# Performance work log

Measured on AMD Instinct MI355X. Metric: run time of the kernel, lower is better.

## Reference

```python
import jax, jax.numpy as jnp
import numpy as np

B, L, H, M = 8, 512, 768, 383
N = M + 1  # +1 dummy epsilon mention
NEG = -10000.0


def _lin(x, W, b):
    return x @ W.T + b


def setup_inputs() -> dict:
    key = jax.random.key(0)
    ks = jax.random.split(key, 26)
    s = 0.02
    inp = {}
    inp["sequence_output"] = jax.random.normal(ks[0], (B, L, H), jnp.float32)
    inp["speaker_emb"] = jax.random.normal(ks[1], (400, H), jnp.float32) * s
    inp["dummy_emb"] = jax.random.normal(ks[2], (1, H), jnp.float32) * s
    inp["W_pair1"] = jax.random.normal(ks[3], (H, 2 * H), jnp.float32) * s
    inp["b_pair1"] = jnp.zeros((H,), jnp.float32)
    inp["W_pair2"] = jax.random.normal(ks[4], (H // 2, H), jnp.float32) * s
    inp["b_pair2"] = jnp.zeros((H // 2,), jnp.float32)
    inp["W_pair3"] = jax.random.normal(ks[5], (1, H // 2), jnp.float32) * s
    inp["b_pair3"] = jnp.zeros((1,), jnp.float32)
    inp["W_m1"] = jax.random.normal(ks[6], (H // 2, H), jnp.float32) * s
    inp["b_m1"] = jnp.zeros((H // 2,), jnp.float32)
    inp["W_m2"] = jax.random.normal(ks[7], (H // 4, H // 2), jnp.float32) * s
    inp["b_m2"] = jnp.zeros((H // 4,), jnp.float32)
    inp["W_m3"] = jax.random.normal(ks[8], (1, H // 4), jnp.float32) * s
    inp["b_m3"] = jnp.zeros((1,), jnp.float32)
    inp["W_c1"] = jax.random.normal(ks[9], (H // 2, H), jnp.float32) * s
    inp["b_c1"] = jnp.zeros((H // 2,), jnp.float32)
    inp["W_c2"] = jax.random.normal(ks[10], (18, H // 2), jnp.float32) * s
    inp["b_c2"] = jnp.zeros((18,), jnp.float32)
    inp["mentions_seg"] = jax.random.randint(ks[11], (M,), 0, B, jnp.int32)
    inp["mention_start"] = jax.random.randint(ks[12], (M,), 0, L, jnp.int32)
    inp["mention_end"] = jax.random.randint(ks[13], (M,), 0, L, jnp.int32)
    inp["speaker_ids"] = jax.random.randint(ks[14], (B, L), 0, 400, jnp.int32)
    second = jnp.arange(1, N, dtype=jnp.int32)  # each real mention is a 'second' exactly once
    first = jax.random.randint(ks[15], (M,), 0, N, jnp.int32) % second  # antecedent strictly before
    inp["link_first"] = first
    inp["link_second"] = second
    inp["character_label"] = jax.random.randint(ks[16], (M,), 0, 18, jnp.int32)
    return inp


def reference(sequence_output, speaker_emb, dummy_emb,
              W_pair1, b_pair1, W_pair2, b_pair2, W_pair3, b_pair3,
              W_m1, b_m1, W_m2, b_m2, W_m3, b_m3,
              W_c1, b_c1, W_c2, b_c2,
              mentions_seg, mention_start, mention_end, speaker_ids,
              link_first, link_second, character_label):
    relu = jax.nn.relu
    # gather mention boundary + speaker reps: [M, H]
    start_rep = sequence_output[mentions_seg, mention_start]
    end_rep = sequence_output[mentions_seg, mention_end]
    spk_rep = speaker_emb[speaker_ids[mentions_seg, mention_start]]
    mention_reps = start_rep + end_rep + spk_rep
    # character linking head: [M, 18]
    char_logits = _lin(relu(_lin(mention_reps, W_c1, b_c1)), W_c2, b_c2)
    # prepend dummy epsilon mention: [N, H]
    all_reps = jnp.concatenate([dummy_emb, mention_reps], axis=0)
    # pairwise MLP; pair[i, j] = MLP(cat(rep_j, rep_i)). Split W_pair1 to avoid [N,N,2H] concat.
    Wa, Wb = W_pair1[:, :H], W_pair1[:, H:]
    A = all_reps @ Wa.T  # contribution of 'first' (column j)
    Bm = all_reps @ Wb.T  # contribution of 'second' (row i)
    h1 = relu(A[None, :, :] + Bm[:, None, :] + b_pair1)  # [N, N, H]
    h2 = relu(jnp.einsum('ijk,hk->ijh', h1, W_pair2) + b_pair2)  # [N, N, H/2]
    pair_scores = jnp.einsum('ijh,oh->ij', h2, W_pair3) + b_pair3[0]  # [N, N]
    # unary mention score: [N]
    ms = (_lin(relu(_lin(relu(_lin(all_reps, W_m1, b_m1)), W_m2, b_m2)), W_m3, b_m3))[:, 0]
    mask = jnp.triu(jnp.ones((N, N), jnp.float32), k=0) * NEG
    mention_scores = pair_scores + ms[None, :] + ms[:, None] + mask
    # linking loss via row-softmax and link gathers
    sm = jax.nn.softmax(mention_scores, axis=1)
    lik = sm[link_second, link_first]  # [num_links]
    col_sum = jnp.zeros((N,), sm.dtype).at[link_second].add(lik)
    nll = -jnp.sum(jnp.log(col_sum[1:]))
    # character cross-entropy (sum reduction)
    logp = jax.nn.log_softmax(char_logits, axis=1)
    ce = -jnp.sum(jnp.take_along_axis(logp, character_label[:, None], axis=1))
    return nll + ce


if __name__ == '__main__':
    out = reference(**setup_inputs())
    print(out)
```

## Files before the change

### kernel.cpp

```cpp
#include <hip/hip_runtime.h>

typedef __bf16 bf16x8 __attribute__((ext_vector_type(8)));
typedef float f32x4 __attribute__((ext_vector_type(4)));

#define WS_S       0
#define WS_ALLREPS 0
#define WS_APRIME  301056
#define WS_BMAT    595968
#define WS_RELUM1  890880
#define WS_RELUC1  1038336
#define WS_MS      1185792
#define WS_W2BF    1186176

#define NPAIR 2352
#define NMS   384
#define NCE   383
#define SLAB  75264

#define SWZ(row,c) (((row)<<2) + ((c) ^ (((row)>>1)&3)))

__device__ __forceinline__ bf16x8 cvt8(float4 a, float4 b) {
  bf16x8 v;
  v[0]=(__bf16)a.x; v[1]=(__bf16)a.y; v[2]=(__bf16)a.z; v[3]=(__bf16)a.w;
  v[4]=(__bf16)b.x; v[5]=(__bf16)b.y; v[6]=(__bf16)b.z; v[7]=(__bf16)b.w;
  return v;
}

__global__ __launch_bounds__(256) void k_build(
    const float* __restrict__ seq, const float* __restrict__ spk_emb,
    const float* __restrict__ dummy, const float* __restrict__ W2,
    const int* __restrict__ seg, const int* __restrict__ mstart,
    const int* __restrict__ mend, const int* __restrict__ spk_ids,
    float* __restrict__ all_reps, __bf16* __restrict__ W2bf,
    float* __restrict__ out) {
  int r = blockIdx.x, t = threadIdx.x;
  if (r < 384) {
    if (r == 0) {
      if (t == 0) out[0] = 0.f;
      #pragma unroll
      for (int e = 0; e < 3; ++e) { int k = t + 256*e; all_reps[k] = dummy[k]; }
    } else {
      int m = r - 1;
      int sg = seg[m], st = mstart[m], en = mend[m];
      int sp = spk_ids[sg*512 + st];
      const float* p1 = seq + (size_t)(sg*512 + st)*768;
      const float* p2 = seq + (size_t)(sg*512 + en)*768;
      const float* p3 = spk_emb + (size_t)sp*768;
      #pragma unroll
      for (int e = 0; e < 3; ++e) { int k = t + 256*e; all_reps[r*768+k] = p1[k]+p2[k]+p3[k]; }
    }
  } else {
    int h = r - 384;
    #pragma unroll
    for (int e = 0; e < 3; ++e) { int k = t + 256*e; W2bf[h*768+k] = (__bf16)W2[h*768+k]; }
  }
}

__global__ __launch_bounds__(256) void k_gemmB(
    const float* __restrict__ reps, const float* __restrict__ W1,
    const float* __restrict__ Wm1, const float* __restrict__ Wc1,
    const float* __restrict__ b1, const float* __restrict__ bm1, const float* __restrict__ bc1,
    float* __restrict__ Aprime, float* __restrict__ Bmat,
    float* __restrict__ relu_m1, float* __restrict__ relu_c1) {
  __shared__ bf16x8 lA[2][256];
  __shared__ bf16x8 lB[2][512];
  int nt = blockIdx.x;
  int m0 = blockIdx.y * 64;
  int t = threadIdx.x;
  const float* src; int stride, coloff;
  if (nt < 6)       { src = W1  + (size_t)(nt*128)*1536;      stride = 1536; coloff = 0;   }
  else if (nt < 12) { src = W1  + (size_t)((nt-6)*128)*1536;  stride = 1536; coloff = 768; }
  else if (nt < 15) { src = Wm1 + (size_t)((nt-12)*128)*768;  stride = 768;  coloff = 0;   }
  else              { src = Wc1 + (size_t)((nt-15)*128)*768;  stride = 768;  coloff = 0;   }

  int w = t>>6, l = t&63;
  int wm = w&1, wn = w>>1;
  int lr = l&15, lg = l>>4;

  int p = t>>2, q = t&3;
  const float* pa  = reps + (size_t)(m0+p)*768 + q*8;
  const float* pb0 = src + (size_t)p*stride + coloff + q*8;
  const float* pb1 = src + (size_t)(p+64)*stride + coloff + q*8;
  int ia  = SWZ(p, q);
  int ib0 = SWZ(p, q);
  int ib1 = SWZ(p+64, q);

  float4 a0, a1, b0, b1v, c0, c1v;
  #define G_LOADG(k0) { \
    a0  = *(const float4*)(pa  + (k0)); a1  = *(const float4*)(pa  + (k0) + 4); \
    b0  = *(const float4*)(pb0 + (k0)); b1v = *(const float4*)(pb0 + (k0) + 4); \
    c0  = *(const float4*)(pb1 + (k0)); c1v = *(const float4*)(pb1 + (k0) + 4); }
  #define G_WRITEB(buf) { \
    lA[buf][ia]  = cvt8(a0, a1); \
    lB[buf][ib0] = cvt8(b0, b1v); \
    lB[buf][ib1] = cvt8(c0, c1v); }

  G_LOADG(0);
  G_WRITEB(0);

  f32x4 acc[2][4] = {};
  int cur = 0;

  for (int ks = 0; ks < 24; ++ks) {
    __syncthreads();
    if (ks < 23) G_LOADG((ks+1)*32);
    bf16x8 af[2], bfr[4];
    #pragma unroll
    for (int fa = 0; fa < 2; ++fa) { int row = wm*32 + fa*16 + lr; af[fa] = lA[cur][SWZ(row, lg)]; }
    #pragma unroll
    for (int fb = 0; fb < 4; ++fb) { int row = wn*64 + fb*16 + lr; bfr[fb] = lB[cur][SWZ(row, lg)]; }
    __builtin_amdgcn_s_setprio(1);
    #pragma unroll
    for (int fa = 0; fa < 2; ++fa)
      #pragma unroll
      for (int fb = 0; fb < 4; ++fb)
        acc[fa][fb] = __builtin_amdgcn_mfma_f32_16x16x32_bf16(af[fa], bfr[fb], acc[fa][fb], 0, 0, 0);
    __builtin_amdgcn_s_setprio(0);
    if (ks < 23) G_WRITEB(cur^1);
    cur ^= 1;
  }

  #pragma unroll
  for (int fa = 0; fa < 2; ++fa) {
    #pragma unroll
    for (int fb = 0; fb < 4; ++fb) {
      #pragma unroll
      for (int reg = 0; reg < 4; ++reg) {
        int m = m0 + wm*32 + fa*16 + lg*4 + reg;
        int nl = wn*64 + fb*16 + lr;
        float v = acc[fa][fb][reg];
        if (nt < 6)       { int n = nt*128 + nl;      Aprime[m*768+n]  = v + b1[n]; }
        else if (nt < 12) { int n = (nt-6)*128 + nl;  Bmat[m*768+n]    = v; }
        else if (nt < 15) { int n = (nt-12)*128 + nl; relu_m1[m*384+n] = fmaxf(v + bm1[n], 0.f); }
        else              { int n = (nt-15)*128 + nl; relu_c1[m*384+n] = fmaxf(v + bc1[n], 0.f); }
      }
    }
  }
}

__global__ __launch_bounds__(128, 2) void k_mega(
    const float* __restrict__ Aprime, const float* __restrict__ Bmat,
    const __bf16* __restrict__ W2bf, const float* __restrict__ b2,
    const float* __restrict__ w3, float* __restrict__ S,
    const float* __restrict__ relu_m1, const float* __restrict__ Wm2,
    const float* __restrict__ bm2, const float* __restrict__ Wm3,
    const float* __restrict__ bm3, float* __restrict__ msv,
    const float* __restrict__ relu_c1, const float* __restrict__ Wc2,
    const float* __restrict__ bc2, const int* __restrict__ label,
    float* __restrict__ out) {
  __shared__ char smem[32768];
  int bx = blockIdx.x, t = threadIdx.x;

  if (bx < NPAIR) {
    bf16x8 (*lA)[256] = (bf16x8 (*)[256])smem;
    bf16x8 (*lB)[768] = (bf16x8 (*)[768])(smem + 8192);
    int tile = bx >> 1, hh = bx & 1;
    int ib = (int)((__fsqrt_rn(8.0f*tile + 1.0f) - 1.0f) * 0.5f);
    while ((ib+1)*(ib+2)/2 <= tile) ++ib;
    while (ib*(ib+1)/2 > tile) --ib;
    int jb = tile - ib*(ib+1)/2;
    int i0 = ib*8, j0 = jb*8;
    int h0 = hh*192;

    int w = t>>6, l = t&63;
    int lr = l&15, lg = l>>4;

    int p = t>>1, qb = (t&1)*2;
    const float* pArow = Aprime + (size_t)(j0 + (p&7))*768 + qb*8;
    const float* pBrow = Bmat   + (size_t)(i0 + (p>>3))*768 + qb*8;
    int idxA0 = SWZ(p, qb), idxA1 = SWZ(p, qb+1);
    const __bf16* pW[6]; int idxW[6];
    #pragma unroll
    for (int e = 0; e < 6; ++e) {
      int c6 = t + 128*e, row = c6>>2, qq = c6&3;
      pW[e] = W2bf + (size_t)(h0 + row)*768 + qq*8;
      idxW[e] = SWZ(row, qq);
    }

    float4 ga0, ga1, ga2, ga3, gb0, gb1, gb2, gb3;
    bf16x8 gw0, gw1, gw2, gw3, gw4, gw5;

    #define LOADG(k0) { \
      ga0 = *(const float4*)(pArow + (k0));     ga1 = *(const float4*)(pArow + (k0) + 4); \
      ga2 = *(const float4*)(pArow + (k0) + 8); ga3 = *(const float4*)(pArow + (k0) + 12); \
      gb0 = *(const float4*)(pBrow + (k0));     gb1 = *(const float4*)(pBrow + (k0) + 4); \
      gb2 = *(const float4*)(pBrow + (k0) + 8); gb3 = *(const float4*)(pBrow + (k0) + 12); \
      gw0 = *(const bf16x8*)(pW[0] + (k0)); gw1 = *(const bf16x8*)(pW[1] + (k0)); \
      gw2 = *(const bf16x8*)(pW[2] + (k0)); gw3 = *(const bf16x8*)(pW[3] + (k0)); \
      gw4 = *(const bf16x8*)(pW[4] + (k0)); gw5 = *(const bf16x8*)(pW[5] + (k0)); }

    #define WRITEB(buf) { \
      float4 r0, r1, r2, r3; \
      r0.x = fmaxf(ga0.x + gb0.x, 0.f); r0.y = fmaxf(ga0.y + gb0.y, 0.f); \
      r0.z = fmaxf(ga0.z + gb0.z, 0.f); r0.w = fmaxf(ga0.w + gb0.w, 0.f); \
      r1.x = fmaxf(ga1.x + gb1.x, 0.f); r1.y = fmaxf(ga1.y + gb1.y, 0.f); \
      r1.z = fmaxf(ga1.z + gb1.z, 0.f); r1.w = fmaxf(ga1.w + gb1.w, 0.f); \
      r2.x = fmaxf(ga2.x + gb2.x, 0.f); r2.y = fmaxf(ga2.y + gb2.y, 0.f); \
      r2.z = fmaxf(ga2.z + gb2.z, 0.f); r2.w = fmaxf(ga2.w + gb2.w, 0.f); \
      r3.x = fmaxf(ga3.x + gb3.x, 0.f); r3.y = fmaxf(ga3.y + gb3.y, 0.f); \
      r3.z = fmaxf(ga3.z + gb3.z, 0.f); r3.w = fmaxf(ga3.w + gb3.w, 0.f); \
      lA[buf][idxA0] = cvt8(r0, r1); \
      lA[buf][idxA1] = cvt8(r2, r3); \
      lB[buf][idxW[0]] = gw0; lB[buf][idxW[1]] = gw1; lB[buf][idxW[2]] = gw2; \
      lB[buf][idxW[3]] = gw3; lB[buf][idxW[4]] = gw4; lB[buf][idxW[5]] = gw5; }

    LOADG(0);
    WRITEB(0);

    f32x4 acc[4][6] = {};
    int cur = 0;

    for (int ks = 0; ks < 24; ++ks) {
      __syncthreads();
      if (ks < 23) LOADG((ks+1)*32);
      bf16x8 af[4], bfr[6];
      #pragma unroll
      for (int fp = 0; fp < 4; ++fp) { int row = fp*16 + lr; af[fp] = lA[cur][SWZ(row, lg)]; }
      #pragma unroll
      for (int fh = 0; fh < 6; ++fh) { int row = w*96 + fh*16 + lr; bfr[fh] = lB[cur][SWZ(row, lg)]; }
      __builtin_amdgcn_s_setprio(1);
      #pragma unroll
      for (int fp = 0; fp < 4; ++fp)
        #pragma unroll
        for (int fh = 0; fh < 6; ++fh)
          acc[fp][fh] = __builtin_amdgcn_mfma_f32_16x16x32_bf16(af[fp], bfr[fh], acc[fp][fh], 0, 0, 0);
      __builtin_amdgcn_s_setprio(0);
      if (ks < 23) WRITEB(cur^1);
      cur ^= 1;
    }

    float sacc[4][4] = {};
    #pragma unroll
    for (int fh = 0; fh < 6; ++fh) {
      int hcol = h0 + w*96 + fh*16 + lr;
      float bb = b2[hcol], ww = w3[hcol];
      #pragma unroll
      for (int fp = 0; fp < 4; ++fp)
        #pragma unroll
        for (int reg = 0; reg < 4; ++reg)
          sacc[fp][reg] += fmaxf(acc[fp][fh][reg] + bb, 0.f) * ww;
    }
    float* Sp = S + (size_t)(hh*2 + w)*SLAB + tile*64;
    #pragma unroll
    for (int fp = 0; fp < 4; ++fp) {
      #pragma unroll
      for (int reg = 0; reg < 4; ++reg) {
        float v = sacc[fp][reg];
        v += __shfl_xor(v, 1); v += __shfl_xor(v, 2);
        v += __shfl_xor(v, 4); v += __shfl_xor(v, 8);
        if (lr == 0) Sp[fp*16 + lg*4 + reg] = v;
      }
    }
  } else if (bx < NPAIR + NMS) {
    float* xs = (float*)smem;
    __shared__ float part[2];
    int r = bx - NPAIR;
    const float4* srcv = (const float4*)(relu_m1 + (size_t)r*384);
    if (t < 96) ((float4*)xs)[t] = srcv[t];
    __syncthreads();
    float d1 = 0.f, d2 = 0.f;
    const float4* w1v = (const float4*)(Wm2 + (size_t)t*384);
    const float4* w2v = (const float4*)(Wm2 + (size_t)(t+128 < 192 ? t+128 : t)*384);
    for (int k = 0; k < 96; ++k) {
      float4 xq = ((const float4*)xs)[k];
      float4 aq = w1v[k];
      d1 += aq.x*xq.x + aq.y*xq.y + aq.z*xq.z + aq.w*xq.w;
      if (t < 64) {
        float4 bq = w2v[k];
        d2 += bq.x*xq.x + bq.y*xq.y + bq.z*xq.z + bq.w*xq.w;
      }
    }
    float c = fmaxf(d1 + bm2[t], 0.f) * Wm3[t];
    if (t < 64) c += fmaxf(d2 + bm2[t+128], 0.f) * Wm3[t+128];
    c += __shfl_xor(c, 1);  c += __shfl_xor(c, 2);  c += __shfl_xor(c, 4);
    c += __shfl_xor(c, 8);  c += __shfl_xor(c, 16); c += __shfl_xor(c, 32);
    if ((t&63) == 0) part[t>>6] = c;
    __syncthreads();
    if (t == 0) msv[r] = part[0] + part[1] + bm3[0];
  } else {
    float* lg = (float*)smem;
    int m = bx - (NPAIR + NMS);
    if (t < 18) {
      const float4* xv = (const float4*)(relu_c1 + (size_t)(m+1)*384);
      const float4* wv = (const float4*)(Wc2 + (size_t)t*384);
      float d = 0.f;
      for (int k = 0; k < 96; ++k) {
        float4 a = xv[k], b = wv[k];
        d += a.x*b.x + a.y*b.y + a.z*b.z + a.w*b.w;
      }
      lg[t] = d + bc2[t];
    }
    __syncthreads();
    if (t == 0) {
      float sum = 0.f;
      for (int c = 0; c < 18; ++c) sum += __expf(lg[c]);
      atomicAdd(out, __logf(sum) - lg[label[m]]);
    }
  }
}

__global__ __launch_bounds__(64) void k_epi(
    const float* __restrict__ S, const float* __restrict__ ms,
    const float* __restrict__ b3, const int* __restrict__ lfirst,
    float* __restrict__ out) {
  int i = blockIdx.x + 1;
  int lane = threadIdx.x;
  int ibb = i >> 3, r = i & 7;
  int f = lfirst[i-1];
  float bb3 = b3[0];
  float esum = 0.f, smf = 0.f;
  int tri = ibb*(ibb+1)/2;
  for (int j = lane; j < i; j += 64) {
    int jbb = j >> 3;
    int idx = (tri + jbb)*64 + r*8 + (j&7);
    float s = S[idx] + S[SLAB + idx] + S[2*SLAB + idx] + S[3*SLAB + idx] + bb3 + ms[j];
    esum += __expf(s);
    if (j == f) smf = s;
  }
  esum += __shfl_xor(esum, 1);  esum += __shfl_xor(esum, 2);
  esum += __shfl_xor(esum, 4);  esum += __shfl_xor(esum, 8);
  esum += __shfl_xor(esum, 16); esum += __shfl_xor(esum, 32);
  smf += __shfl_xor(smf, 1);  smf += __shfl_xor(smf, 2);
  smf += __shfl_xor(smf, 4);  smf += __shfl_xor(smf, 8);
  smf += __shfl_xor(smf, 16); smf += __shfl_xor(smf, 32);
  if (lane == 0) atomicAdd(out, __logf(esum) - smf);
}

extern "C" void kernel_launch(void* const* d_in, const int* in_sizes, int n_in,
                              void* d_out, int out_size, void* d_ws, size_t ws_size,
                              hipStream_t stream) {
  (void)in_sizes; (void)n_in; (void)out_size; (void)ws_size;
  const float* seq   = (const float*)d_in[0];
  const float* spk   = (const float*)d_in[1];
  const float* dummy = (const float*)d_in[2];
  const float* W1    = (const float*)d_in[3];
  const float* b1    = (const float*)d_in[4];
  const float* W2    = (const float*)d_in[5];
  const float* b2    = (const float*)d_in[6];
  const float* W3    = (const float*)d_in[7];
  const float* b3    = (const float*)d_in[8];
  const float* Wm1   = (const float*)d_in[9];
  const float* bm1   = (const float*)d_in[10];
  const float* Wm2   = (const float*)d_in[11];
  const float* bm2   = (const float*)d_in[12];
  const float* Wm3   = (const float*)d_in[13];
  const float* bm3   = (const float*)d_in[14];
  const float* Wc1   = (const float*)d_in[15];
  const float* bc1   = (const float*)d_in[16];
  const float* Wc2   = (const float*)d_in[17];
  const float* bc2   = (const float*)d_in[18];
  const int* seg     = (const int*)d_in[19];
  const int* mstart  = (const int*)d_in[20];
  const int* mend    = (const int*)d_in[21];
  const int* spk_ids = (const int*)d_in[22];
  const int* lfirst  = (const int*)d_in[23];
  const int* clabel  = (const int*)d_in[25];

  float* ws = (float*)d_ws;
  float* S        = ws + WS_S;
  float* all_reps = ws + WS_ALLREPS;
  float* Aprime   = ws + WS_APRIME;
  float* Bmat     = ws + WS_BMAT;
  float* relu_m1  = ws + WS_RELUM1;
  float* relu_c1  = ws + WS_RELUC1;
  float* msv      = ws + WS_MS;
  __bf16* W2bf    = (__bf16*)(ws + WS_W2BF);
  float* out      = (float*)d_out;

  k_build<<<768, 256, 0, stream>>>(seq, spk, dummy, W2, seg, mstart, mend, spk_ids, all_reps, W2bf, out);
  k_gemmB<<<dim3(18,6), 256, 0, stream>>>(all_reps, W1, Wm1, Wc1, b1, bm1, bc1, Aprime, Bmat, relu_m1, relu_c1);
  k_mega<<<NPAIR + NMS + NCE, 128, 0, stream>>>(Aprime, Bmat, W2bf, b2, W3, S,
                                                relu_m1, Wm2, bm2, Wm3, bm3, msv,
                                                relu_c1, Wc2, bc2, clabel, out);
  k_epi<<<383, 64, 0, stream>>>(S, msv, b3, lfirst, out);
}
```

Baseline: 240.2 us.

## Enlarge pair tiles to 16x8, prepermute W2 and stage it via direct-to-LDS loads

The pair-scoring kernel moves to 256-thread blocks covering 16 'second' rows by 8 'first' rows, roughly halving the block count. Each W2 slice staged in LDS is now reused across twice as many pair rows, and the partial scores are reduced in shared memory, so only two S slabs reach global memory instead of four. W2 is pre-permuted into a swizzled bf16 layout in k_build, letting the kernel stream it straight into LDS with global_load_lds instead of through registers. The unary mention-score blocks now handle two mentions each, and the small blocks are moved to the front of the grid. In exchange LDS use per block rises and the triangular tile mapping and epilogue indexing get more complex.

```diff
diff --git a/kernel.cpp b/kernel.cpp
--- a/kernel.cpp
+++ b/kernel.cpp
@@ -10,12 +10,13 @@
 #define WS_RELUM1  890880
 #define WS_RELUC1  1038336
 #define WS_MS      1185792
-#define WS_W2BF    1186176
-
-#define NPAIR 2352
-#define NMS   384
+#define WS_W2PERM  1186176
+
+#define NMSB  192
 #define NCE   383
-#define SLAB  75264
+#define PAIRBASE 575
+#define NPAIR 1200
+#define SLAB  76800
 
 #define SWZ(row,c) (((row)<<2) + ((c) ^ (((row)>>1)&3)))
 
@@ -26,12 +27,18 @@
   return v;
 }
 
+__device__ __forceinline__ void gload_lds16(const void* g, void* l) {
+  __builtin_amdgcn_global_load_lds(
+      (const __attribute__((address_space(1))) void*)g,
+      (__attribute__((address_space(3))) void*)l, 16, 0, 0);
+}
+
 __global__ __launch_bounds__(256) void k_build(
     const float* __restrict__ seq, const float* __restrict__ spk_emb,
     const float* __restrict__ dummy, const float* __restrict__ W2,
     const int* __restrict__ seg, const int* __restrict__ mstart,
     const int* __restrict__ mend, const int* __restrict__ spk_ids,
-    float* __restrict__ all_reps, __bf16* __restrict__ W2bf,
+    float* __restrict__ all_reps, __bf16* __restrict__ W2perm,
     float* __restrict__ out) {
   int r = blockIdx.x, t = threadIdx.x;
   if (r < 384) {
@@ -50,9 +57,18 @@
       for (int e = 0; e < 3; ++e) { int k = t + 256*e; all_reps[r*768+k] = p1[k]+p2[k]+p3[k]; }
     }
   } else {
-    int h = r - 384;
-    #pragma unroll
-    for (int e = 0; e < 3; ++e) { int k = t + 256*e; W2bf[h*768+k] = (__bf16)W2[h*768+k]; }
+    int idx = r - 384, hhb = idx / 24, ksb = idx % 24;
+    bf16x8* dst = (bf16x8*)W2perm + (size_t)(hhb*24 + ksb)*768;
+    #pragma unroll
+    for (int e = 0; e < 3; ++e) {
+      int u = t + 256*e;
+      int row = u >> 2;
+      int q = (u & 3) ^ ((u >> 3) & 3);
+      const float* sp = W2 + (size_t)(hhb*192 + row)*768 + ksb*32 + q*8;
+      float4 f0 = *(const float4*)sp;
+      float4 f1 = *(const float4*)(sp + 4);
+      dst[u] = cvt8(f0, f1);
+    }
   }
 }
 
@@ -138,9 +154,9 @@
   }
 }
 
-__global__ __launch_bounds__(128, 2) void k_mega(
+__global__ __launch_bounds__(256, 2) void k_mega(
     const float* __restrict__ Aprime, const float* __restrict__ Bmat,
-    const __bf16* __restrict__ W2bf, const float* __restrict__ b2,
+    const __bf16* __restrict__ W2perm, const float* __restrict__ b2,
     const float* __restrict__ w3, float* __restrict__ S,
     const float* __restrict__ relu_m1, const float* __restrict__ Wm2,
     const float* __restrict__ bm2, const float* __restrict__ Wm3,
@@ -148,48 +164,63 @@
     const float* __restrict__ relu_c1, const float* __restrict__ Wc2,
     const float* __restrict__ bc2, const int* __restrict__ label,
     float* __restrict__ out) {
-  __shared__ char smem[32768];
+  __shared__ char smem[41984];
+  __shared__ float part[2][4];
   int bx = blockIdx.x, t = threadIdx.x;
 
-  if (bx < NPAIR) {
-    bf16x8 (*lA)[256] = (bf16x8 (*)[256])smem;
-    bf16x8 (*lB)[768] = (bf16x8 (*)[768])(smem + 8192);
-    int tile = bx >> 1, hh = bx & 1;
-    int ib = (int)((__fsqrt_rn(8.0f*tile + 1.0f) - 1.0f) * 0.5f);
-    while ((ib+1)*(ib+2)/2 <= tile) ++ib;
-    while (ib*(ib+1)/2 > tile) --ib;
-    int jb = tile - ib*(ib+1)/2;
-    int i0 = ib*8, j0 = jb*8;
-    int h0 = hh*192;
+  if (bx >= PAIRBASE) {
+    bf16x8 (*lA)[512] = (bf16x8 (*)[512])smem;
+    bf16x8 (*lB)[768] = (bf16x8 (*)[768])(smem + 16384);
+    float  (*score)[2] = (float (*)[2])(smem + 40960);
+    int pb = bx - PAIRBASE;
+    int tile = pb >> 1, hh = pb & 1;
+    int ib = (int)((__fsqrt_rn(4.0f*tile + 1.0f) - 1.0f) * 0.5f);
+    while ((ib+1)*(ib+2) <= tile) ++ib;
+    while (ib*(ib+1) > tile) --ib;
+    int jb = tile - ib*(ib+1);
+    int i0 = ib*16, j0 = jb*8;
 
     int w = t>>6, l = t&63;
+    int wp = w&1, wh = w>>1;
     int lr = l&15, lg = l>>4;
 
     int p = t>>1, qb = (t&1)*2;
     const float* pArow = Aprime + (size_t)(j0 + (p&7))*768 + qb*8;
     const float* pBrow = Bmat   + (size_t)(i0 + (p>>3))*768 + qb*8;
     int idxA0 = SWZ(p, qb), idxA1 = SWZ(p, qb+1);
-    const __bf16* pW[6]; int idxW[6];
-    #pragma unroll
-    for (int e = 0; e < 6; ++e) {
-      int c6 = t + 128*e, row = c6>>2, qq = c6&3;
-      pW[e] = W2bf + (size_t)(h0 + row)*768 + qq*8;
-      idxW[e] = SWZ(row, qq);
-    }
-
-    float4 ga0, ga1, ga2, ga3, gb0, gb1, gb2, gb3;
-    bf16x8 gw0, gw1, gw2, gw3, gw4, gw5;
-
-    #define LOADG(k0) { \
+    const bf16x8* wsrc = (const bf16x8*)W2perm + (size_t)hh*24*768;
+    int wbase = t & 192;
+
+    float4 ga0, ga1, gb0, gb1;
+
+    #define LOADG_A(k0) { \
+      ga0 = *(const float4*)(pArow + (k0)); ga1 = *(const float4*)(pArow + (k0) + 4); \
+      gb0 = *(const float4*)(pBrow + (k0)); gb1 = *(const float4*)(pBrow + (k0) + 4); }
+
+    #define STAGE_B(ksv, buf) { \
+      const bf16x8* gs = wsrc + (size_t)(ksv)*768; \
+      gload_lds16(gs +       t, &lB[buf][      wbase]); \
+      gload_lds16(gs + 256 + t, &lB[buf][256 + wbase]); \
+      gload_lds16(gs + 512 + t, &lB[buf][512 + wbase]); }
+
+    #define WRITEB_A(buf) { \
+      float4 r0, r1; \
+      r0.x = fmaxf(ga0.x + gb0.x, 0.f); r0.y = fmaxf(ga0.y + gb0.y, 0.f); \
+      r0.z = fmaxf(ga0.z + gb0.z, 0.f); r0.w = fmaxf(ga0.w + gb0.w, 0.f); \
+      r1.x = fmaxf(ga1.x + gb1.x, 0.f); r1.y = fmaxf(ga1.y + gb1.y, 0.f); \
+      r1.z = fmaxf(ga1.z + gb1.z, 0.f); r1.w = fmaxf(ga1.w + gb1.w, 0.f); \
+      bf16x8 h01 = cvt8(r0, r1); \
+      if ((t&1) == 0) lA[buf][idxA0] = h01; else lA[buf][idxA1] = h01; }
+
+    float4 ga2, ga3, gb2, gb3;
+    #undef LOADG_A
+    #define LOADG_A(k0) { \
       ga0 = *(const float4*)(pArow + (k0));     ga1 = *(const float4*)(pArow + (k0) + 4); \
       ga2 = *(const float4*)(pArow + (k0) + 8); ga3 = *(const float4*)(pArow + (k0) + 12); \
       gb0 = *(const float4*)(pBrow + (k0));     gb1 = *(const float4*)(pBrow + (k0) + 4); \
-      gb2 = *(const float4*)(pBrow + (k0) + 8); gb3 = *(const float4*)(pBrow + (k0) + 12); \
-      gw0 = *(const bf16x8*)(pW[0] + (k0)); gw1 = *(const bf16x8*)(pW[1] + (k0)); \
-      gw2 = *(const bf16x8*)(pW[2] + (k0)); gw3 = *(const bf16x8*)(pW[3] + (k0)); \
-      gw4 = *(const bf16x8*)(pW[4] + (k0)); gw5 = *(const bf16x8*)(pW[5] + (k0)); }
-
-    #define WRITEB(buf) { \
+      gb2 = *(const float4*)(pBrow + (k0) + 8); gb3 = *(const float4*)(pBrow + (k0) + 12); }
+    #undef WRITEB_A
+    #define WRITEB_A(buf) { \
       float4 r0, r1, r2, r3; \
       r0.x = fmaxf(ga0.x + gb0.x, 0.f); r0.y = fmaxf(ga0.y + gb0.y, 0.f); \
       r0.z = fmaxf(ga0.z + gb0.z, 0.f); r0.w = fmaxf(ga0.w + gb0.w, 0.f); \
@@ -200,24 +231,23 @@
       r3.x = fmaxf(ga3.x + gb3.x, 0.f); r3.y = fmaxf(ga3.y + gb3.y, 0.f); \
       r3.z = fmaxf(ga3.z + gb3.z, 0.f); r3.w = fmaxf(ga3.w + gb3.w, 0.f); \
       lA[buf][idxA0] = cvt8(r0, r1); \
-      lA[buf][idxA1] = cvt8(r2, r3); \
-      lB[buf][idxW[0]] = gw0; lB[buf][idxW[1]] = gw1; lB[buf][idxW[2]] = gw2; \
-      lB[buf][idxW[3]] = gw3; lB[buf][idxW[4]] = gw4; lB[buf][idxW[5]] = gw5; }
-
-    LOADG(0);
-    WRITEB(0);
+      lA[buf][idxA1] = cvt8(r2, r3); }
+
+    LOADG_A(0);
+    STAGE_B(0, 0);
+    WRITEB_A(0);
 
     f32x4 acc[4][6] = {};
     int cur = 0;
 
     for (int ks = 0; ks < 24; ++ks) {
       __syncthreads();
-      if (ks < 23) LOADG((ks+1)*32);
+      if (ks < 23) { STAGE_B(ks+1, cur^1); LOADG_A((ks+1)*32); }
       bf16x8 af[4], bfr[6];
       #pragma unroll
-      for (int fp = 0; fp < 4; ++fp) { int row = fp*16 + lr; af[fp] = lA[cur][SWZ(row, lg)]; }
-      #pragma unroll
-      for (int fh = 0; fh < 6; ++fh) { int row = w*96 + fh*16 + lr; bfr[fh] = lB[cur][SWZ(row, lg)]; }
+      for (int fp = 0; fp < 4; ++fp) { int row = wp*64 + fp*16 + lr; af[fp] = lA[cur][SWZ(row, lg)]; }
+      #pragma unroll
+      for (int fh = 0; fh < 6; ++fh) { int row = wh*96 + fh*16 + lr; bfr[fh] = lB[cur][SWZ(row, lg)]; }
       __builtin_amdgcn_s_setprio(1);
       #pragma unroll
       for (int fp = 0; fp < 4; ++fp)
@@ -225,14 +255,14 @@
         for (int fh = 0; fh < 6; ++fh)
           acc[fp][fh] = __builtin_amdgcn_mfma_f32_16x16x32_bf16(af[fp], bfr[fh], acc[fp][fh], 0, 0, 0);
       __builtin_amdgcn_s_setprio(0);
-      if (ks < 23) WRITEB(cur^1);
+      if (ks < 23) WRITEB_A(cur^1);
       cur ^= 1;
     }
 
     float sacc[4][4] = {};
     #pragma unroll
     for (int fh = 0; fh < 6; ++fh) {
-      int hcol = h0 + w*96 + fh*16 + lr;
+      int hcol = hh*192 + wh*96 + fh*16 + lr;
       float bb = b2[hcol], ww = w3[hcol];
       #pragma unroll
       for (int fp = 0; fp < 4; ++fp)
@@ -240,7 +270,6 @@
         for (int reg = 0; reg < 4; ++reg)
           sacc[fp][reg] += fmaxf(acc[fp][fh][reg] + bb, 0.f) * ww;
     }
-    float* Sp = S + (size_t)(hh*2 + w)*SLAB + tile*64;
     #pragma unroll
     for (int fp = 0; fp < 4; ++fp) {
       #pragma unroll
@@ -248,38 +277,42 @@
         float v = sacc[fp][reg];
         v += __shfl_xor(v, 1); v += __shfl_xor(v, 2);
         v += __shfl_xor(v, 4); v += __shfl_xor(v, 8);
-        if (lr == 0) Sp[fp*16 + lg*4 + reg] = v;
+        if (lr == 0) score[wp*64 + fp*16 + lg*4 + reg][wh] = v;
       }
     }
-  } else if (bx < NPAIR + NMS) {
+    __syncthreads();
+    if (t < 128) S[(size_t)hh*SLAB + tile*128 + t] = score[t][0] + score[t][1];
+  } else if (bx < NMSB) {
     float* xs = (float*)smem;
-    __shared__ float part[2];
-    int r = bx - NPAIR;
-    const float4* srcv = (const float4*)(relu_m1 + (size_t)r*384);
-    if (t < 96) ((float4*)xs)[t] = srcv[t];
+    int r0 = bx*2;
+    const float4* srcv = (const float4*)(relu_m1 + (size_t)r0*384);
+    if (t < 192) ((float4*)xs)[t] = srcv[t];
     __syncthreads();
-    float d1 = 0.f, d2 = 0.f;
-    const float4* w1v = (const float4*)(Wm2 + (size_t)t*384);
-    const float4* w2v = (const float4*)(Wm2 + (size_t)(t+128 < 192 ? t+128 : t)*384);
-    for (int k = 0; k < 96; ++k) {
-      float4 xq = ((const float4*)xs)[k];
-      float4 aq = w1v[k];
-      d1 += aq.x*xq.x + aq.y*xq.y + aq.z*xq.z + aq.w*xq.w;
-      if (t < 64) {
-        float4 bq = w2v[k];
-        d2 += bq.x*xq.x + bq.y*xq.y + bq.z*xq.z + bq.w*xq.w;
+    float a[2] = {};
+    if (t < 192) {
+      const float4* wv = (const float4*)(Wm2 + (size_t)t*384);
+      for (int k = 0; k < 96; ++k) {
+        float4 wq = wv[k];
+        #pragma unroll
+        for (int rr = 0; rr < 2; ++rr) {
+          float4 xq = *(const float4*)&xs[rr*384 + k*4];
+          a[rr] += wq.x*xq.x + wq.y*xq.y + wq.z*xq.z + wq.w*xq.w;
+        }
       }
     }
-    float c = fmaxf(d1 + bm2[t], 0.f) * Wm3[t];
-    if (t < 64) c += fmaxf(d2 + bm2[t+128], 0.f) * Wm3[t+128];
-    c += __shfl_xor(c, 1);  c += __shfl_xor(c, 2);  c += __shfl_xor(c, 4);
-    c += __shfl_xor(c, 8);  c += __shfl_xor(c, 16); c += __shfl_xor(c, 32);
-    if ((t&63) == 0) part[t>>6] = c;
+    float wm3 = (t < 192) ? Wm3[t] : 0.f, bb = (t < 192) ? bm2[t] : 0.f;
+    #pragma unroll
+    for (int rr = 0; rr < 2; ++rr) {
+      float c = (t < 192) ? fmaxf(a[rr] + bb, 0.f) * wm3 : 0.f;
+      c += __shfl_xor(c, 1);  c += __shfl_xor(c, 2);  c += __shfl_xor(c, 4);
+      c += __shfl_xor(c, 8);  c += __shfl_xor(c, 16); c += __shfl_xor(c, 32);
+      if ((t&63) == 0) part[rr][t>>6] = c;
+    }
     __syncthreads();
-    if (t == 0) msv[r] = part[0] + part[1] + bm3[0];
+    if (t < 2) msv[r0+t] = part[t][0] + part[t][1] + part[t][2] + part[t][3] + bm3[0];
   } else {
     float* lg = (float*)smem;
-    int m = bx - (NPAIR + NMS);
+    int m = bx - NMSB;
     if (t < 18) {
       const float4* xv = (const float4*)(relu_c1 + (size_t)(m+1)*384);
       const float4* wv = (const float4*)(Wc2 + (size_t)t*384);
@@ -305,15 +338,15 @@
     float* __restrict__ out) {
   int i = blockIdx.x + 1;
   int lane = threadIdx.x;
-  int ibb = i >> 3, r = i & 7;
+  int ibb = i >> 4, r = i & 15;
   int f = lfirst[i-1];
   float bb3 = b3[0];
   float esum = 0.f, smf = 0.f;
-  int tri = ibb*(ibb+1)/2;
+  int tri = ibb*(ibb+1);
   for (int j = lane; j < i; j += 64) {
     int jbb = j >> 3;
-    int idx = (tri + jbb)*64 + r*8 + (j&7);
-    float s = S[idx] + S[SLAB + idx] + S[2*SLAB + idx] + S[3*SLAB + idx] + bb3 + ms[j];
+    int idx = (tri + jbb)*128 + r*8 + (j&7);
+    float s = S[idx] + S[SLAB + idx] + bb3 + ms[j];
     esum += __expf(s);
     if (j == f) smf = s;
   }
@@ -364,13 +397,13 @@
   float* relu_m1  = ws + WS_RELUM1;
   float* relu_c1  = ws + WS_RELUC1;
   float* msv      = ws + WS_MS;
-  __bf16* W2bf    = (__bf16*)(ws + WS_W2BF);
+  __bf16* W2perm  = (__bf16*)(ws + WS_W2PERM);
   float* out      = (float*)d_out;
 
-  k_build<<<768, 256, 0, stream>>>(seq, spk, dummy, W2, seg, mstart, mend, spk_ids, all_reps, W2bf, out);
+  k_build<<<432, 256, 0, stream>>>(seq, spk, dummy, W2, seg, mstart, mend, spk_ids, all_reps, W2perm, out);
   k_gemmB<<<dim3(18,6), 256, 0, stream>>>(all_reps, W1, Wm1, Wc1, b1, bm1, bc1, Aprime, Bmat, relu_m1, relu_c1);
-  k_mega<<<NPAIR + NMS + NCE, 128, 0, stream>>>(Aprime, Bmat, W2bf, b2, W3, S,
-                                                relu_m1, Wm2, bm2, Wm3, bm3, msv,
-                                                relu_c1, Wc2, bc2, clabel, out);
+  k_mega<<<PAIRBASE + NPAIR, 256, 0, stream>>>(Aprime, Bmat, W2perm, b2, W3, S,
+                                               relu_m1, Wm2, bm2, Wm3, bm3, msv,
+                                               relu_c1, Wc2, bc2, clabel, out);
   k_epi<<<383, 64, 0, stream>>>(S, msv, b3, lfirst, out);
 }
```

Measured after the change: 251.4 us. 1.05x slower.

## Fuse mention build into gemm, retile pair kernel into three H-slices

Applied to the files above, without the earlier changes.

Removes the separate build kernel. Mention representations are now gathered and summed directly inside the first GEMM's load stage, and the W2 bf16 conversion runs in extra blocks of the same launch. The pair-scoring kernel switches from 128-thread blocks covering 192 hidden columns to 256-thread blocks covering 128 columns, split three ways. Partial scores are reduced in shared memory, so the epilogue sums three slabs instead of four. Unary-score blocks now process two rows each, and the small blocks are scheduled before the pair blocks. The trade-off is that the gather is recomputed per column tile, and there are more pair blocks, each reusing less data.

```diff
diff --git a/kernel.cpp b/kernel.cpp
--- a/kernel.cpp
+++ b/kernel.cpp
@@ -4,7 +4,6 @@
 typedef float f32x4 __attribute__((ext_vector_type(4)));
 
 #define WS_S       0
-#define WS_ALLREPS 0
 #define WS_APRIME  301056
 #define WS_BMAT    595968
 #define WS_RELUM1  890880
@@ -12,9 +11,11 @@
 #define WS_MS      1185792
 #define WS_W2BF    1186176
 
-#define NPAIR 2352
-#define NMS   384
+#define NMSB  192
 #define NCE   383
+#define PAIRBASE 575
+#define NTILE 1176
+#define NPAIRB 3528
 #define SLAB  75264
 
 #define SWZ(row,c) (((row)<<2) + ((c) ^ (((row)>>1)&3)))
@@ -26,47 +27,35 @@
   return v;
 }
 
-__global__ __launch_bounds__(256) void k_build(
+__global__ __launch_bounds__(256) void k_gb(
     const float* __restrict__ seq, const float* __restrict__ spk_emb,
     const float* __restrict__ dummy, const float* __restrict__ W2,
     const int* __restrict__ seg, const int* __restrict__ mstart,
     const int* __restrict__ mend, const int* __restrict__ spk_ids,
-    float* __restrict__ all_reps, __bf16* __restrict__ W2bf,
-    float* __restrict__ out) {
-  int r = blockIdx.x, t = threadIdx.x;
-  if (r < 384) {
-    if (r == 0) {
-      if (t == 0) out[0] = 0.f;
-      #pragma unroll
-      for (int e = 0; e < 3; ++e) { int k = t + 256*e; all_reps[k] = dummy[k]; }
-    } else {
-      int m = r - 1;
-      int sg = seg[m], st = mstart[m], en = mend[m];
-      int sp = spk_ids[sg*512 + st];
-      const float* p1 = seq + (size_t)(sg*512 + st)*768;
-      const float* p2 = seq + (size_t)(sg*512 + en)*768;
-      const float* p3 = spk_emb + (size_t)sp*768;
-      #pragma unroll
-      for (int e = 0; e < 3; ++e) { int k = t + 256*e; all_reps[r*768+k] = p1[k]+p2[k]+p3[k]; }
-    }
-  } else {
-    int h = r - 384;
-    #pragma unroll
-    for (int e = 0; e < 3; ++e) { int k = t + 256*e; W2bf[h*768+k] = (__bf16)W2[h*768+k]; }
-  }
-}
-
-__global__ __launch_bounds__(256) void k_gemmB(
-    const float* __restrict__ reps, const float* __restrict__ W1,
+    const float* __restrict__ W1,
     const float* __restrict__ Wm1, const float* __restrict__ Wc1,
     const float* __restrict__ b1, const float* __restrict__ bm1, const float* __restrict__ bc1,
     float* __restrict__ Aprime, float* __restrict__ Bmat,
-    float* __restrict__ relu_m1, float* __restrict__ relu_c1) {
+    float* __restrict__ relu_m1, float* __restrict__ relu_c1,
+    __bf16* __restrict__ W2bf, float* __restrict__ out) {
+  int bx = blockIdx.x, t = threadIdx.x;
+
+  if (bx >= 108) {
+    int r = bx - 108;
+    if (r == 0 && t == 0) out[0] = 0.f;
+    #pragma unroll
+    for (int rr = 0; rr < 8; ++rr) {
+      int base = (r*8 + rr)*768;
+      #pragma unroll
+      for (int e = 0; e < 3; ++e) { int k = t + 256*e; W2bf[base+k] = (__bf16)W2[base+k]; }
+    }
+    return;
+  }
+
   __shared__ bf16x8 lA[2][256];
   __shared__ bf16x8 lB[2][512];
-  int nt = blockIdx.x;
-  int m0 = blockIdx.y * 64;
-  int t = threadIdx.x;
+  int nt = bx % 18;
+  int m0 = (bx / 18) * 64;
   const float* src; int stride, coloff;
   if (nt < 6)       { src = W1  + (size_t)(nt*128)*1536;      stride = 1536; coloff = 0;   }
   else if (nt < 12) { src = W1  + (size_t)((nt-6)*128)*1536;  stride = 1536; coloff = 768; }
@@ -78,7 +67,18 @@
   int lr = l&15, lg = l>>4;
 
   int p = t>>2, q = t&3;
-  const float* pa  = reps + (size_t)(m0+p)*768 + q*8;
+  int row = m0 + p;
+  const float *pa1, *pa2, *pa3;
+  bool rz = (row == 0);
+  if (rz) { pa1 = dummy + q*8; pa2 = pa1; pa3 = pa1; }
+  else {
+    int m = row - 1;
+    int sg = seg[m], st = mstart[m], en = mend[m];
+    int sp = spk_ids[sg*512 + st];
+    pa1 = seq + (size_t)(sg*512 + st)*768 + q*8;
+    pa2 = seq + (size_t)(sg*512 + en)*768 + q*8;
+    pa3 = spk_emb + (size_t)sp*768 + q*8;
+  }
   const float* pb0 = src + (size_t)p*stride + coloff + q*8;
   const float* pb1 = src + (size_t)(p+64)*stride + coloff + q*8;
   int ia  = SWZ(p, q);
@@ -87,7 +87,13 @@
 
   float4 a0, a1, b0, b1v, c0, c1v;
   #define G_LOADG(k0) { \
-    a0  = *(const float4*)(pa  + (k0)); a1  = *(const float4*)(pa  + (k0) + 4); \
+    float4 x0 = *(const float4*)(pa1 + (k0)), x1 = *(const float4*)(pa1 + (k0) + 4); \
+    float4 y0 = *(const float4*)(pa2 + (k0)), y1 = *(const float4*)(pa2 + (k0) + 4); \
+    float4 z0 = *(const float4*)(pa3 + (k0)), z1 = *(const float4*)(pa3 + (k0) + 4); \
+    if (rz) { a0 = x0; a1 = x1; } \
+    else { \
+      a0.x = x0.x+y0.x+z0.x; a0.y = x0.y+y0.y+z0.y; a0.z = x0.z+y0.z+z0.z; a0.w = x0.w+y0.w+z0.w; \
+      a1.x = x1.x+y1.x+z1.x; a1.y = x1.y+y1.y+z1.y; a1.z = x1.z+y1.z+z1.z; a1.w = x1.w+y1.w+z1.w; } \
     b0  = *(const float4*)(pb0 + (k0)); b1v = *(const float4*)(pb0 + (k0) + 4); \
     c0  = *(const float4*)(pb1 + (k0)); c1v = *(const float4*)(pb1 + (k0) + 4); }
   #define G_WRITEB(buf) { \
@@ -106,9 +112,9 @@
     if (ks < 23) G_LOADG((ks+1)*32);
     bf16x8 af[2], bfr[4];
     #pragma unroll
-    for (int fa = 0; fa < 2; ++fa) { int row = wm*32 + fa*16 + lr; af[fa] = lA[cur][SWZ(row, lg)]; }
-    #pragma unroll
-    for (int fb = 0; fb < 4; ++fb) { int row = wn*64 + fb*16 + lr; bfr[fb] = lB[cur][SWZ(row, lg)]; }
+    for (int fa = 0; fa < 2; ++fa) { int rr = wm*32 + fa*16 + lr; af[fa] = lA[cur][SWZ(rr, lg)]; }
+    #pragma unroll
+    for (int fb = 0; fb < 4; ++fb) { int rr = wn*64 + fb*16 + lr; bfr[fb] = lB[cur][SWZ(rr, lg)]; }
     __builtin_amdgcn_s_setprio(1);
     #pragma unroll
     for (int fa = 0; fa < 2; ++fa)
@@ -138,7 +144,7 @@
   }
 }
 
-__global__ __launch_bounds__(128, 2) void k_mega(
+__global__ __launch_bounds__(256, 4) void k_mega(
     const float* __restrict__ Aprime, const float* __restrict__ Bmat,
     const __bf16* __restrict__ W2bf, const float* __restrict__ b2,
     const float* __restrict__ w3, float* __restrict__ S,
@@ -148,138 +154,132 @@
     const float* __restrict__ relu_c1, const float* __restrict__ Wc2,
     const float* __restrict__ bc2, const int* __restrict__ label,
     float* __restrict__ out) {
-  __shared__ char smem[32768];
+  __shared__ char smem[25088];
+  __shared__ float part[2][4];
   int bx = blockIdx.x, t = threadIdx.x;
 
-  if (bx < NPAIR) {
+  if (bx >= PAIRBASE) {
     bf16x8 (*lA)[256] = (bf16x8 (*)[256])smem;
-    bf16x8 (*lB)[768] = (bf16x8 (*)[768])(smem + 8192);
-    int tile = bx >> 1, hh = bx & 1;
-    int ib = (int)((__fsqrt_rn(8.0f*tile + 1.0f) - 1.0f) * 0.5f);
-    while ((ib+1)*(ib+2)/2 <= tile) ++ib;
-    while (ib*(ib+1)/2 > tile) --ib;
-    int jb = tile - ib*(ib+1)/2;
-    int i0 = ib*8, j0 = jb*8;
-    int h0 = hh*192;
+    bf16x8 (*lB)[512] = (bf16x8 (*)[512])(smem + 8192);
+    float  (*score)[2] = (float (*)[2])(smem + 24576);
+    int pb = bx - PAIRBASE;
+    int tt = pb / 3, hh = pb - tt*3;
+    int ib = (int)((__fsqrt_rn(8.0f*tt + 1.0f) - 1.0f) * 0.5f);
+    while ((ib+1)*(ib+2)/2 <= tt) ++ib;
+    while (ib*(ib+1)/2 > tt) --ib;
+    int jb = tt - ib*(ib+1)/2;
+    int i0 = ib*8, j0 = jb*8, h0 = hh*128;
 
     int w = t>>6, l = t&63;
+    int wp = w&1, wh = w>>1;
     int lr = l&15, lg = l>>4;
 
-    int p = t>>1, qb = (t&1)*2;
-    const float* pArow = Aprime + (size_t)(j0 + (p&7))*768 + qb*8;
-    const float* pBrow = Bmat   + (size_t)(i0 + (p>>3))*768 + qb*8;
-    int idxA0 = SWZ(p, qb), idxA1 = SWZ(p, qb+1);
-    const __bf16* pW[6]; int idxW[6];
-    #pragma unroll
-    for (int e = 0; e < 6; ++e) {
-      int c6 = t + 128*e, row = c6>>2, qq = c6&3;
-      pW[e] = W2bf + (size_t)(h0 + row)*768 + qq*8;
-      idxW[e] = SWZ(row, qq);
-    }
-
-    float4 ga0, ga1, ga2, ga3, gb0, gb1, gb2, gb3;
-    bf16x8 gw0, gw1, gw2, gw3, gw4, gw5;
+    int p = t>>2, q = t&3;
+    const float* pArow = Aprime + (size_t)(j0 + (p&7))*768 + q*8;
+    const float* pBrow = Bmat   + (size_t)(i0 + (p>>3))*768 + q*8;
+    int idxA = SWZ(p, q);
+    const __bf16* pW0; const __bf16* pW1; int idxW0, idxW1;
+    { int u0 = t, u1 = t + 256;
+      pW0 = W2bf + (size_t)(h0 + (u0>>2))*768 + (u0&3)*8;
+      pW1 = W2bf + (size_t)(h0 + (u1>>2))*768 + (u1&3)*8;
+      idxW0 = SWZ(u0>>2, u0&3); idxW1 = SWZ(u1>>2, u1&3); }
+
+    float4 ga0, ga1, gb0, gb1;
+    bf16x8 gw0, gw1;
 
     #define LOADG(k0) { \
-      ga0 = *(const float4*)(pArow + (k0));     ga1 = *(const float4*)(pArow + (k0) + 4); \
-      ga2 = *(const float4*)(pArow + (k0) + 8); ga3 = *(const float4*)(pArow + (k0) + 12); \
-      gb0 = *(const float4*)(pBrow + (k0));     gb1 = *(const float4*)(pBrow + (k0) + 4); \
-      gb2 = *(const float4*)(pBrow + (k0) + 8); gb3 = *(const float4*)(pBrow + (k0) + 12); \
-      gw0 = *(const bf16x8*)(pW[0] + (k0)); gw1 = *(const bf16x8*)(pW[1] + (k0)); \
-      gw2 = *(const bf16x8*)(pW[2] + (k0)); gw3 = *(const bf16x8*)(pW[3] + (k0)); \
-      gw4 = *(const bf16x8*)(pW[4] + (k0)); gw5 = *(const bf16x8*)(pW[5] + (k0)); }
+      ga0 = *(const float4*)(pArow + (k0)); ga1 = *(const float4*)(pArow + (k0) + 4); \
+      gb0 = *(const float4*)(pBrow + (k0)); gb1 = *(const float4*)(pBrow + (k0) + 4); \
+      gw0 = *(const bf16x8*)(pW0 + (k0));   gw1 = *(const bf16x8*)(pW1 + (k0)); }
 
     #define WRITEB(buf) { \
-      float4 r0, r1, r2, r3; \
+      float4 r0, r1; \
       r0.x = fmaxf(ga0.x + gb0.x, 0.f); r0.y = fmaxf(ga0.y + gb0.y, 0.f); \
       r0.z = fmaxf(ga0.z + gb0.z, 0.f); r0.w = fmaxf(ga0.w + gb0.w, 0.f); \
       r1.x = fmaxf(ga1.x + gb1.x, 0.f); r1.y = fmaxf(ga1.y + gb1.y, 0.f); \
       r1.z = fmaxf(ga1.z + gb1.z, 0.f); r1.w = fmaxf(ga1.w + gb1.w, 0.f); \
-      r2.x = fmaxf(ga2.x + gb2.x, 0.f); r2.y = fmaxf(ga2.y + gb2.y, 0.f); \
-      r2.z = fmaxf(ga2.z + gb2.z, 0.f); r2.w = fmaxf(ga2.w + gb2.w, 0.f); \
-      r3.x = fmaxf(ga3.x + gb3.x, 0.f); r3.y = fmaxf(ga3.y + gb3.y, 0.f); \
-      r3.z = fmaxf(ga3.z + gb3.z, 0.f); r3.w = fmaxf(ga3.w + gb3.w, 0.f); \
-      lA[buf][idxA0] = cvt8(r0, r1); \
-      lA[buf][idxA1] = cvt8(r2, r3); \
-      lB[buf][idxW[0]] = gw0; lB[buf][idxW[1]] = gw1; lB[buf][idxW[2]] = gw2; \
-      lB[buf][idxW[3]] = gw3; lB[buf][idxW[4]] = gw4; lB[buf][idxW[5]] = gw5; }
+      lA[buf][idxA] = cvt8(r0, r1); \
+      lB[buf][idxW0] = gw0; lB[buf][idxW1] = gw1; }
 
     LOADG(0);
     WRITEB(0);
 
-    f32x4 acc[4][6] = {};
+    f32x4 acc[2][4] = {};
     int cur = 0;
 
     for (int ks = 0; ks < 24; ++ks) {
       __syncthreads();
       if (ks < 23) LOADG((ks+1)*32);
-      bf16x8 af[4], bfr[6];
-      #pragma unroll
-      for (int fp = 0; fp < 4; ++fp) { int row = fp*16 + lr; af[fp] = lA[cur][SWZ(row, lg)]; }
-      #pragma unroll
-      for (int fh = 0; fh < 6; ++fh) { int row = w*96 + fh*16 + lr; bfr[fh] = lB[cur][SWZ(row, lg)]; }
+      bf16x8 af[2], bfr[4];
+      #pragma unroll
+      for (int fp = 0; fp < 2; ++fp) { int rr = wp*32 + fp*16 + lr; af[fp] = lA[cur][SWZ(rr, lg)]; }
+      #pragma unroll
+      for (int fh = 0; fh < 4; ++fh) { int rr = wh*64 + fh*16 + lr; bfr[fh] = lB[cur][SWZ(rr, lg)]; }
       __builtin_amdgcn_s_setprio(1);
       #pragma unroll
-      for (int fp = 0; fp < 4; ++fp)
+      for (int fp = 0; fp < 2; ++fp)
         #pragma unroll
-        for (int fh = 0; fh < 6; ++fh)
+        for (int fh = 0; fh < 4; ++fh)
           acc[fp][fh] = __builtin_amdgcn_mfma_f32_16x16x32_bf16(af[fp], bfr[fh], acc[fp][fh], 0, 0, 0);
       __builtin_amdgcn_s_setprio(0);
       if (ks < 23) WRITEB(cur^1);
       cur ^= 1;
     }
 
-    float sacc[4][4] = {};
-    #pragma unroll
-    for (int fh = 0; fh < 6; ++fh) {
-      int hcol = h0 + w*96 + fh*16 + lr;
+    float sacc[2][4] = {};
+    #pragma unroll
+    for (int fh = 0; fh < 4; ++fh) {
+      int hcol = h0 + wh*64 + fh*16 + lr;
       float bb = b2[hcol], ww = w3[hcol];
       #pragma unroll
-      for (int fp = 0; fp < 4; ++fp)
+      for (int fp = 0; fp < 2; ++fp)
         #pragma unroll
         for (int reg = 0; reg < 4; ++reg)
           sacc[fp][reg] += fmaxf(acc[fp][fh][reg] + bb, 0.f) * ww;
     }
-    float* Sp = S + (size_t)(hh*2 + w)*SLAB + tile*64;
-    #pragma unroll
-    for (int fp = 0; fp < 4; ++fp) {
+    #pragma unroll
+    for (int fp = 0; fp < 2; ++fp) {
       #pragma unroll
       for (int reg = 0; reg < 4; ++reg) {
         float v = sacc[fp][reg];
         v += __shfl_xor(v, 1); v += __shfl_xor(v, 2);
         v += __shfl_xor(v, 4); v += __shfl_xor(v, 8);
-        if (lr == 0) Sp[fp*16 + lg*4 + reg] = v;
+        if (lr == 0) score[wp*32 + fp*16 + lg*4 + reg][wh] = v;
       }
     }
-  } else if (bx < NPAIR + NMS) {
+    __syncthreads();
+    if (t < 64) S[(size_t)hh*SLAB + tt*64 + t] = score[t][0] + score[t][1];
+  } else if (bx < NMSB) {
     float* xs = (float*)smem;
-    __shared__ float part[2];
-    int r = bx - NPAIR;
-    const float4* srcv = (const float4*)(relu_m1 + (size_t)r*384);
-    if (t < 96) ((float4*)xs)[t] = srcv[t];
-    __syncthreads();
-    float d1 = 0.f, d2 = 0.f;
-    const float4* w1v = (const float4*)(Wm2 + (size_t)t*384);
-    const float4* w2v = (const float4*)(Wm2 + (size_t)(t+128 < 192 ? t+128 : t)*384);
-    for (int k = 0; k < 96; ++k) {
-      float4 xq = ((const float4*)xs)[k];
-      float4 aq = w1v[k];
-      d1 += aq.x*xq.x + aq.y*xq.y + aq.z*xq.z + aq.w*xq.w;
-      if (t < 64) {
-        float4 bq = w2v[k];
-        d2 += bq.x*xq.x + bq.y*xq.y + bq.z*xq.z + bq.w*xq.w;
+    int r0 = bx*2;
+    const float4* srcv = (const float4*)(relu_m1 + (size_t)r0*384);
+    if (t < 192) ((float4*)xs)[t] = srcv[t];
+    __syncthreads();
+    float a[2] = {};
+    if (t < 192) {
+      const float4* wv = (const float4*)(Wm2 + (size_t)t*384);
+      for (int k = 0; k < 96; ++k) {
+        float4 wq = wv[k];
+        #pragma unroll
+        for (int rr = 0; rr < 2; ++rr) {
+          float4 xq = *(const float4*)&xs[rr*384 + k*4];
+          a[rr] += wq.x*xq.x + wq.y*xq.y + wq.z*xq.z + wq.w*xq.w;
+        }
       }
     }
-    float c = fmaxf(d1 + bm2[t], 0.f) * Wm3[t];
-    if (t < 64) c += fmaxf(d2 + bm2[t+128], 0.f) * Wm3[t+128];
-    c += __shfl_xor(c, 1);  c += __shfl_xor(c, 2);  c += __shfl_xor(c, 4);
-    c += __shfl_xor(c, 8);  c += __shfl_xor(c, 16); c += __shfl_xor(c, 32);
-    if ((t&63) == 0) part[t>>6] = c;
-    __syncthreads();
-    if (t == 0) msv[r] = part[0] + part[1] + bm3[0];
+    float wm3 = (t < 192) ? Wm3[t] : 0.f, bb = (t < 192) ? bm2[t] : 0.f;
+    #pragma unroll
+    for (int rr = 0; rr < 2; ++rr) {
+      float c = (t < 192) ? fmaxf(a[rr] + bb, 0.f) * wm3 : 0.f;
+      c += __shfl_xor(c, 1);  c += __shfl_xor(c, 2);  c += __shfl_xor(c, 4);
+      c += __shfl_xor(c, 8);  c += __shfl_xor(c, 16); c += __shfl_xor(c, 32);
+      if ((t&63) == 0) part[rr][t>>6] = c;
+    }
+    __syncthreads();
+    if (t < 2) msv[r0+t] = part[t][0] + part[t][1] + part[t][2] + part[t][3] + bm3[0];
   } else {
     float* lg = (float*)smem;
-    int m = bx - (NPAIR + NMS);
+    int m = bx - NMSB;
     if (t < 18) {
       const float4* xv = (const float4*)(relu_c1 + (size_t)(m+1)*384);
       const float4* wv = (const float4*)(Wc2 + (size_t)t*384);
@@ -313,7 +313,7 @@
   for (int j = lane; j < i; j += 64) {
     int jbb = j >> 3;
     int idx = (tri + jbb)*64 + r*8 + (j&7);
-    float s = S[idx] + S[SLAB + idx] + S[2*SLAB + idx] + S[3*SLAB + idx] + bb3 + ms[j];
+    float s = S[idx] + S[SLAB + idx] + S[2*SLAB + idx] + bb3 + ms[j];
     esum += __expf(s);
     if (j == f) smf = s;
   }
@@ -358,7 +358,6 @@
 
   float* ws = (float*)d_ws;
   float* S        = ws + WS_S;
-  float* all_reps = ws + WS_ALLREPS;
   float* Aprime   = ws + WS_APRIME;
   float* Bmat     = ws + WS_BMAT;
   float* relu_m1  = ws + WS_RELUM1;
@@ -367,9 +366,10 @@
   __bf16* W2bf    = (__bf16*)(ws + WS_W2BF);
   float* out      = (float*)d_out;
 
-  k_build<<<768, 256, 0, stream>>>(seq, spk, dummy, W2, seg, mstart, mend, spk_ids, all_reps, W2bf, out);
-  k_gemmB<<<dim3(18,6), 256, 0, stream>>>(all_reps, W1, Wm1, Wc1, b1, bm1, bc1, Aprime, Bmat, relu_m1, relu_c1);
-  k_mega<<<NPAIR + NMS + NCE, 128, 0, stream>>>(Aprime, Bmat, W2bf, b2, W3, S,
+  k_gb<<<156, 256, 0, stream>>>(seq, spk, dummy, W2, seg, mstart, mend, spk_ids,
+                                W1, Wm1, Wc1, b1, bm1, bc1,
+                                Aprime, Bmat, relu_m1, relu_c1, W2bf, out);
+  k_mega<<<PAIRBASE + NPAIRB, 256, 0, stream>>>(Aprime, Bmat, W2bf, b2, W3, S,
                                                 relu_m1, Wm2, bm2, Wm3, bm3, msv,
                                                 relu_c1, Wc2, bc2, clabel, out);
   k_epi<<<383, 64, 0, stream>>>(S, msv, b3, lfirst, out);
```

Measured after the change: 234.9 us. 1.02x faster.
